# Kernel optimization log

Measured on AMD Instinct MI355X. Metric: run time of the kernel, lower is better.

The kernel has to match this reference:

```python
import jax, jax.numpy as jnp
import numpy as np

SCALE = 10.0
THRESH = 1e-3   # nn.Threshold(eps, 0)
NORM_EPS = 1e-12  # F.normalize default eps
LEAKY_SLOPE = 0.01


def _proj(x, W1, W2):
    # x: [B, C, L]; conv1x1 == channel matmul
    h = jnp.einsum('oc,bcl->bol', W1, x)
    h = jnp.where(h >= 0, h, LEAKY_SLOPE * h)
    return jnp.einsum('oc,bcl->bol', W2, h)


def _l2norm(x):
    # normalize over channel dim (dim=1), torch F.normalize semantics
    n = jnp.sqrt(jnp.sum(x * x, axis=1, keepdims=True))
    return x / jnp.maximum(n, NORM_EPS)


def setup_inputs() -> dict:
    key = jax.random.key(0)
    k1, k2, k3, k4 = jax.random.split(key, 4)
    B, C, L, OUT = 4, 64, 4096, 64
    query = jax.random.normal(k1, (B, C, L), dtype=jnp.float32)
    kv = jax.random.normal(k2, (B, C, L), dtype=jnp.float32)
    W1 = jax.random.normal(k3, (2 * C, C), dtype=jnp.float32) * (1.0 / np.sqrt(C))
    W2 = jax.random.normal(k4, (OUT, 2 * C), dtype=jnp.float32) * (1.0 / np.sqrt(2 * C))
    return {"query": query, "key": kv, "W1": W1, "W2": W2}


def reference(query, key, W1, W2):
    # self_attention=True: query_conv is key_conv (shared weights)
    q = _l2norm(_proj(query, W1, W2))   # [B, O, L]
    k = _l2norm(_proj(key, W1, W2))     # [B, O, L]
    scores = jnp.einsum('bcl,bcm->blm', q, k) * SCALE  # [B, L, L]
    w = jax.nn.softmax(scores, axis=-1)
    return jnp.where(w > THRESH, w, 0.0)
```

## Files before the change

### kernel.cpp

```cpp
#include <hip/hip_runtime.h>
#include <math.h>

#define B 4
#define C 64
#define L 4096
#define OUTC 64
#define SCALE 10.0f
#define THRESH 1e-3f

#define NS 18
#define SCOLS (NS * 128)
#define EROW 2308
#define SMEM_E_BYTES (16 * EROW * 2)
#define SMEM_WSUM_OFF SMEM_E_BYTES
#define SMEM_RINV_OFF (SMEM_E_BYTES + 512)
#define SMEM_BYTES (SMEM_E_BYTES + 512 + 64)

typedef float v4f __attribute__((ext_vector_type(4)));
typedef short bf16x8 __attribute__((ext_vector_type(8)));
typedef unsigned short us8 __attribute__((ext_vector_type(8)));
typedef unsigned short us4 __attribute__((ext_vector_type(4)));

__device__ __forceinline__ unsigned short f2bf(float x) {
    unsigned int u = __float_as_uint(x);
    u += 0x7fffu + ((u >> 16) & 1u);
    return (unsigned short)(u >> 16);
}
__device__ __forceinline__ float bf2f(unsigned short h) {
    return __uint_as_float(((unsigned int)h) << 16);
}
__device__ __forceinline__ v4f mfma16(bf16x8 a, bf16x8 b, v4f c) {
    return __builtin_amdgcn_mfma_f32_16x16x32_bf16(a, b, c, 0, 0, 0);
}


__global__ void __launch_bounds__(256) proj_kernel(
    const float* __restrict__ q_in, const float* __restrict__ k_in,
    const float* __restrict__ W1, const float* __restrict__ W2,
    unsigned short* __restrict__ Qh, unsigned short* __restrict__ Ql,
    unsigned short* __restrict__ Kh, unsigned short* __restrict__ Kl)
{
    int bid   = blockIdx.x;
    int xcd   = bid & 7;
    int b     = xcd >> 1;
    int which = (bid >> 3) & 1;
    int lt    = ((bid >> 4) << 1) | (xcd & 1);
    int l0    = lt << 6;
    int t     = threadIdx.x;
    int g     = t >> 6;
    int l     = t & 63;

    const float* __restrict__ src =
        (which ? k_in : q_in) + (size_t)b * C * L + l0 + l;
    unsigned short* __restrict__ dh = which ? Kh : Qh;
    unsigned short* __restrict__ dl = which ? Kl : Ql;

    __shared__ float Ht[128][65];
    __shared__ float red[4][64];

    float xr[C];
    #pragma unroll
    for (int c = 0; c < C; ++c)
        xr[c] = src[(size_t)c * L];

    #pragma unroll 1
    for (int oo = 0; oo < 32; oo += 4) {
        #pragma unroll
        for (int u = 0; u < 4; ++u) {
            int o = g * 32 + oo + u;
            float h0 = 0.f, h1 = 0.f, h2 = 0.f, h3 = 0.f;
            #pragma unroll
            for (int c = 0; c < C; c += 4) {
                h0 = fmaf(W1[o * C + c + 0], xr[c + 0], h0);
                h1 = fmaf(W1[o * C + c + 1], xr[c + 1], h1);
                h2 = fmaf(W1[o * C + c + 2], xr[c + 2], h2);
                h3 = fmaf(W1[o * C + c + 3], xr[c + 3], h3);
            }
            float h = (h0 + h1) + (h2 + h3);
            Ht[o][l] = (h >= 0.0f) ? h : 0.01f * h;
        }
    }
    __syncthreads();

    float y[16];
    #pragma unroll
    for (int u = 0; u < 16; ++u) y[u] = 0.f;

    #pragma unroll 1
    for (int hh = 0; hh < 2 * C; hh += 16) {
        float hr[16];
        #pragma unroll
        for (int r = 0; r < 16; ++r)
            hr[r] = Ht[hh + r][l];
        #pragma unroll
        for (int u = 0; u < 16; ++u) {
            int o = g * 16 + u;
            #pragma unroll
            for (int h = 0; h < 16; ++h)
                y[u] = fmaf(W2[o * (2 * C) + hh + h], hr[h], y[u]);
        }
    }

    float ss = 0.f;
    #pragma unroll
    for (int u = 0; u < 16; ++u) ss = fmaf(y[u], y[u], ss);
    red[g][l] = ss;
    __syncthreads();
    float tot = red[0][l] + red[1][l] + red[2][l] + red[3][l];
    float inv = 1.0f / fmaxf(sqrtf(tot), 1e-12f);

    unsigned short hs[16], ls[16];
    #pragma unroll
    for (int u = 0; u < 16; ++u) {
        float val = y[u] * inv;
        hs[u] = f2bf(val);
        ls[u] = f2bf(val - bf2f(hs[u]));
    }
    {
        int col   = l0 + l;
        int tile  = col >> 4;
        int lnn   = col & 15;
        int chunk = g >> 1;
        int quad0 = (g & 1) * 2;
        size_t base0 = (((size_t)b * 256 + tile) * 2 + chunk) * 512
                     + (size_t)(quad0 * 16 + lnn) * 8;
        size_t base1 = base0 + 128;
        *(us8*)(dh + base0) = *(us8*)&hs[0];
        *(us8*)(dh + base1) = *(us8*)&hs[8];
        *(us8*)(dl + base0) = *(us8*)&ls[0];
        *(us8*)(dl + base1) = *(us8*)&ls[8];
    }
}

#define LOADK(TILE) do {                                                 \
    size_t _kb = ((ktb + (size_t)(TILE)) * 2) * 512 + (size_t)lane * 8;  \
    kh0 = *(const bf16x8*)(Kh + _kb);                                    \
    kl0 = *(const bf16x8*)(Kl + _kb);                                    \
    kh1 = *(const bf16x8*)(Kh + _kb + 512);                              \
    kl1 = *(const bf16x8*)(Kl + _kb + 512);                              \
} while (0)

#define DOMFMA() do {                                                    \
    acc = (v4f){0.f, 0.f, 0.f, 0.f};                                     \
    acc = mfma16(aQ[0][0], kh0, acc);                                    \
    acc = mfma16(aQ[0][1], kh0, acc);                                    \
    acc = mfma16(aQ[0][0], kl0, acc);                                    \
    acc = mfma16(aQ[1][0], kh1, acc);                                    \
    acc = mfma16(aQ[1][1], kh1, acc);                                    \
    acc = mfma16(aQ[1][0], kl1, acc);                                    \
} while (0)

__global__ void __launch_bounds__(512) scores_kernel(
    const unsigned short* __restrict__ Qh, const unsigned short* __restrict__ Ql,
    const unsigned short* __restrict__ Kh, const unsigned short* __restrict__ Kl,
    float* __restrict__ out)
{
    extern __shared__ unsigned char smem[];
    unsigned short* __restrict__ e_t  = (unsigned short*)smem;
    float*          __restrict__ wsum = (float*)(smem + SMEM_WSUM_OFF);
    float*          __restrict__ rinv = (float*)(smem + SMEM_RINV_OFF);

    int bid  = blockIdx.x;
    int xcd  = bid & 7;
    int b    = xcd >> 1;
    int r0   = (((bid >> 3) << 1) | (xcd & 1)) << 4;
    int t    = threadIdx.x;
    int wave = t >> 6;
    int lane = t & 63;
    int quad = lane >> 4;
    int ln   = lane & 15;
    int wave16ln = wave * 16 + ln;
    int rowbase  = quad * 4;

    bf16x8 aQ[2][2];
    {
        size_t rowtile = (size_t)b * 256 + (r0 >> 4);
        #pragma unroll
        for (int c0 = 0; c0 < 2; ++c0) {
            size_t base = (rowtile * 2 + c0) * 512 + (size_t)lane * 8;
            aQ[c0][0] = *(const bf16x8*)(Qh + base);
            aQ[c0][1] = *(const bf16x8*)(Ql + base);
        }
    }

    const size_t ktb = (size_t)b * 256;
    bf16x8 kh0, kl0, kh1, kl1;
    v4f acc;
    v4f ps = (v4f){0.f, 0.f, 0.f, 0.f};

    #pragma unroll 2
    for (int i = 0; i < NS; ++i) {
        LOADK(i * 8 + wave);
        DOMFMA();
        #pragma unroll
        for (int r = 0; r < 4; ++r) {
            float ev = __expf(fmaf(SCALE, acc[r], -SCALE));
            ps[r] += ev;
            e_t[(rowbase + r) * EROW + i * 128 + wave16ln] =
                __builtin_bit_cast(unsigned short, (_Float16)ev);
        }
    }
    #pragma unroll 2
    for (int i = NS; i < 32; ++i) {
        LOADK(i * 8 + wave);
        DOMFMA();
        #pragma unroll
        for (int r = 0; r < 4; ++r)
            ps[r] += __expf(fmaf(SCALE, acc[r], -SCALE));
    }

    #pragma unroll
    for (int r = 0; r < 4; ++r) {
        float s = ps[r];
        s += __shfl_xor(s, 1);
        s += __shfl_xor(s, 2);
        s += __shfl_xor(s, 4);
        s += __shfl_xor(s, 8);
        if (ln == 0) wsum[(rowbase + r) * 8 + wave] = s;
    }
    __syncthreads();
    if (t < 16) {
        float s = 0.f;
        #pragma unroll
        for (int w = 0; w < 8; ++w) s += wsum[t * 8 + w];
        rinv[t] = 1.0f / s;
    }
    __syncthreads();

    float rv[4];
    #pragma unroll
    for (int r = 0; r < 4; ++r)
        rv[r] = rinv[rowbase + r];

    float* __restrict__ outb = out + ((size_t)b * L + r0) * L;

    #pragma unroll 2
    for (int i = NS; i < 32; ++i) {
        LOADK(i * 8 + wave);
        DOMFMA();
        int col = i * 128 + wave16ln;
        #pragma unroll
        for (int r = 0; r < 4; ++r) {
            float w = __expf(fmaf(SCALE, acc[r], -SCALE)) * rv[r];
            w = (w > THRESH) ? w : 0.f;
            __builtin_nontemporal_store(
                w, outb + (size_t)(rowbase + r) * L + col);
        }
    }

    {
        int row = t >> 5;
        int c0  = (t & 31) * 4;
        float ri = rinv[row];
        const unsigned short* __restrict__ erow = e_t + (size_t)row * EROW;
        float* __restrict__ orow = outb + (size_t)row * L;

        #pragma unroll 2
        for (int it = 0; it < NS; ++it) {
            int col = it * 128 + c0;
            us4 hv = *(const us4*)(erow + col);
            v4f o;
            #pragma unroll
            for (int j = 0; j < 4; ++j) {
                float w = (float)__builtin_bit_cast(_Float16,
                                                    (unsigned short)hv[j]) * ri;
                o[j] = (w > THRESH) ? w : 0.f;
            }
            __builtin_nontemporal_store(o, (v4f*)(orow + col));
        }
    }
}

extern "C" void kernel_launch(void* const* d_in, const int* in_sizes, int n_in,
                              void* d_out, int out_size, void* d_ws, size_t ws_size,
                              hipStream_t stream) {
    const float* query = (const float*)d_in[0];
    const float* key   = (const float*)d_in[1];
    const float* W1    = (const float*)d_in[2];
    const float* W2    = (const float*)d_in[3];
    float* out = (float*)d_out;

    unsigned short* Qh = (unsigned short*)d_ws;
    unsigned short* Ql = Qh + (size_t)B * L * OUTC;
    unsigned short* Kh = Ql + (size_t)B * L * OUTC;
    unsigned short* Kl = Kh + (size_t)B * L * OUTC;

    hipLaunchKernelGGL(proj_kernel, dim3(512), dim3(256), 0, stream,
                       query, key, W1, W2, Qh, Ql, Kh, Kl);
    hipLaunchKernelGGL(scores_kernel, dim3(1024), dim3(512), SMEM_BYTES, stream,
                       Qh, Ql, Kh, Kl, out);
}
```

Before: 385.1 us.

## Stage recomputed score tiles through LDS for vectorized output stores; shrink cached split

The recompute phase now writes each 16x128 probability tile into a double-buffered shared-memory transpose buffer and then issues 16-byte coalesced row-wise nontemporal stores, replacing scattered scalar stores. To make room for this buffer, the number of column tiles cached as fp16 in LDS drops from 18 to 15, so more tiles are recomputed with MFMA. The change adds a block barrier per tile and extra recompute work in exchange for wider, more coalesced global writes.

```diff
diff --git a/kernel.cpp b/kernel.cpp
--- a/kernel.cpp
+++ b/kernel.cpp
@@ -8,13 +8,15 @@
 #define SCALE 10.0f
 #define THRESH 1e-3f
 
-#define NS 18
+#define NS 15
 #define SCOLS (NS * 128)
-#define EROW 2308
+#define EROW (SCOLS + 4)
 #define SMEM_E_BYTES (16 * EROW * 2)
-#define SMEM_WSUM_OFF SMEM_E_BYTES
-#define SMEM_RINV_OFF (SMEM_E_BYTES + 512)
-#define SMEM_BYTES (SMEM_E_BYTES + 512 + 64)
+#define SMEM_PT_OFF  SMEM_E_BYTES
+#define SMEM_PT_BYTES (2 * 16 * 132 * 4)
+#define SMEM_WSUM_OFF (SMEM_PT_OFF + SMEM_PT_BYTES)
+#define SMEM_RINV_OFF (SMEM_WSUM_OFF + 512)
+#define SMEM_BYTES (SMEM_RINV_OFF + 64)
 
 typedef float v4f __attribute__((ext_vector_type(4)));
 typedef short bf16x8 __attribute__((ext_vector_type(8)));
@@ -157,6 +159,7 @@
 {
     extern __shared__ unsigned char smem[];
     unsigned short* __restrict__ e_t  = (unsigned short*)smem;
+    float*          __restrict__ Pt   = (float*)(smem + SMEM_PT_OFF);
     float*          __restrict__ wsum = (float*)(smem + SMEM_WSUM_OFF);
     float*          __restrict__ rinv = (float*)(smem + SMEM_RINV_OFF);
 
@@ -233,31 +236,35 @@
         rv[r] = rinv[rowbase + r];
 
     float* __restrict__ outb = out + ((size_t)b * L + r0) * L;
-
-    #pragma unroll 2
-    for (int i = NS; i < 32; ++i) {
-        LOADK(i * 8 + wave);
+    int srow = t >> 5;
+    int scol = (t & 31) * 4;
+
+    #pragma unroll 1
+    for (int T = NS; T < 32; ++T) {
+        int buf = T & 1;
+        LOADK(T * 8 + wave);
         DOMFMA();
-        int col = i * 128 + wave16ln;
         #pragma unroll
         for (int r = 0; r < 4; ++r) {
             float w = __expf(fmaf(SCALE, acc[r], -SCALE)) * rv[r];
             w = (w > THRESH) ? w : 0.f;
-            __builtin_nontemporal_store(
-                w, outb + (size_t)(rowbase + r) * L + col);
-        }
+            Pt[(buf * 16 + rowbase + r) * 132 + wave16ln] = w;
+        }
+        __syncthreads();
+
+        v4f o = *(const v4f*)&Pt[(buf * 16 + srow) * 132 + scol];
+        __builtin_nontemporal_store(
+            o, (v4f*)(outb + (size_t)srow * L + T * 128 + scol));
     }
 
     {
-        int row = t >> 5;
-        int c0  = (t & 31) * 4;
-        float ri = rinv[row];
-        const unsigned short* __restrict__ erow = e_t + (size_t)row * EROW;
-        float* __restrict__ orow = outb + (size_t)row * L;
+        float ri = rinv[srow];
+        const unsigned short* __restrict__ erow = e_t + (size_t)srow * EROW;
+        float* __restrict__ orow = outb + (size_t)srow * L;
 
         #pragma unroll 2
         for (int it = 0; it < NS; ++it) {
-            int col = it * 128 + c0;
+            int col = it * 128 + scol;
             us4 hv = *(const us4*)(erow + col);
             v4f o;
             #pragma unroll
```

New measurement: 404.0 us. +4.9%, slower.
